# Kernel optimization log

Measured on AMD Instinct MI355X. Metric: run time of the kernel, lower is better.

The kernel has to match this reference:

```python
import jax, jax.numpy as jnp
import numpy as np

D_MODEL = 2048
NUM_Q_HEADS = 32
NUM_KV_HEADS = 8
HEAD_DIM = D_MODEL // NUM_Q_HEADS  # 64
DIM_KV = NUM_KV_HEADS * HEAD_DIM   # 512
ROPE_THETA = 500000.0
B, T = 1, 2048


def setup_inputs() -> dict:
    key = jax.random.key(0)
    ks = jax.random.split(key, 7)
    f = lambda k, shape, scale: (jax.random.normal(k, shape, jnp.float32) * scale)
    return {
        "q_embs": f(ks[0], (B, T, D_MODEL), 1.0),
        "k_embs": f(ks[1], (B, T, D_MODEL), 1.0),
        "v_embs": f(ks[2], (B, T, D_MODEL), 1.0),
        "w_q": f(ks[3], (D_MODEL, D_MODEL), 0.02),
        "w_k": f(ks[4], (D_MODEL, DIM_KV), 0.02),
        "w_v": f(ks[5], (D_MODEL, DIM_KV), 0.02),
        "w_o": f(ks[6], (D_MODEL, D_MODEL), 0.02),
    }


def _rope(x):
    # x: (B, H, T, D). Llama-style interleaved rotary embedding.
    Tn, D = x.shape[-2], x.shape[-1]
    inv_freq = 1.0 / (ROPE_THETA ** (jnp.arange(0, D, 2, dtype=jnp.float32) / D))  # (D/2,)
    ang = jnp.arange(Tn, dtype=jnp.float32)[:, None] * inv_freq[None, :]  # (T, D/2)
    cos, sin = jnp.cos(ang), jnp.sin(ang)
    x1, x2 = x[..., ::2], x[..., 1::2]
    # interleave rotated pairs back into last dim
    out = jnp.stack([x1 * cos - x2 * sin, x1 * sin + x2 * cos], axis=-1)
    return out.reshape(x.shape)


def reference(q_embs, k_embs, v_embs, w_q, w_k, w_v, w_o):
    Bn, Tn, _ = q_embs.shape
    # projections, then split heads: (B, T, H*D) -> (B, H, T, D)
    q = (q_embs @ w_q).reshape(Bn, Tn, NUM_Q_HEADS, HEAD_DIM).transpose(0, 2, 1, 3)
    k = (k_embs @ w_k).reshape(Bn, Tn, NUM_KV_HEADS, HEAD_DIM).transpose(0, 2, 1, 3)
    v = (v_embs @ w_v).reshape(Bn, Tn, NUM_KV_HEADS, HEAD_DIM).transpose(0, 2, 1, 3)
    q = _rope(q)
    k = _rope(k)
    # GQA: repeat each kv head n_rep consecutive times (matches torch expand+rearrange)
    n_rep = NUM_Q_HEADS // NUM_KV_HEADS
    k = jnp.repeat(k, n_rep, axis=1)
    v = jnp.repeat(v, n_rep, axis=1)
    scores = jnp.einsum("bhqd,bhkd->bhqk", q, k) * (HEAD_DIM ** -0.5)
    causal = jnp.tril(jnp.ones((Tn, Tn), dtype=bool))
    scores = jnp.where(causal, scores, -jnp.inf)
    wei = jax.nn.softmax(scores, axis=-1)
    out = jnp.einsum("bhqk,bhkd->bhqd", wei, v)
    out = out.transpose(0, 2, 1, 3).reshape(Bn, Tn, NUM_Q_HEADS * HEAD_DIM)
    return out @ w_o
```

## Files before the change

### kernel.cpp

```cpp
#include <hip/hip_runtime.h>
#include <hip/hip_bf16.h>
#include <cstdint>

#define D_MODEL 2048
#define T_SEQ   2048
#define NQH     32
#define NKVH    8
#define HD      64
#define DIM_KV  512

typedef __attribute__((ext_vector_type(8))) __bf16 bf16x8;
typedef __attribute__((ext_vector_type(4))) float  f32x4;
typedef __attribute__((ext_vector_type(4))) unsigned int u32x4;
typedef unsigned short ushort_t;

#define NEG_BIG (-1e30f)
#define AS1 __attribute__((address_space(1)))
#define AS3 __attribute__((address_space(3)))

__device__ __forceinline__ float bf2f(unsigned int u) {
    union { unsigned int i; float f; } v; v.i = u << 16; return v.f;
}
__device__ __forceinline__ ushort_t f2bf(float f) {
    __hip_bfloat16 h = __float2bfloat16(f);
    return *reinterpret_cast<ushort_t*>(&h);
}
__device__ __forceinline__ void gll16(const ushort_t* g, ushort_t* l) {
    __builtin_amdgcn_global_load_lds((const AS1 void*)g, (AS3 void*)l, 16, 0, 0);
}

__global__ __launch_bounds__(256) void conv_bf16(const float* __restrict__ X,
                                                 ushort_t* __restrict__ E, int n) {
    int i8 = (blockIdx.x * 256 + threadIdx.x) * 8;
    if (i8 >= n) return;
    f32x4 a = *(const f32x4*)(X + i8);
    f32x4 b = *(const f32x4*)(X + i8 + 4);
    u32x4 r;
    r.x = (unsigned)f2bf(a.x) | ((unsigned)f2bf(a.y) << 16);
    r.y = (unsigned)f2bf(a.z) | ((unsigned)f2bf(a.w) << 16);
    r.z = (unsigned)f2bf(b.x) | ((unsigned)f2bf(b.y) << 16);
    r.w = (unsigned)f2bf(b.z) | ((unsigned)f2bf(b.w) << 16);
    *(u32x4*)(E + i8) = r;
}

__global__ __launch_bounds__(256) void transpose_w(const float* __restrict__ W,
                                                   ushort_t* __restrict__ Wt,
                                                   int K, int N) {
    __shared__ ushort_t tile[64][65];
    int n0 = blockIdx.x * 64;
    int k0 = blockIdx.y * 64;
    int tid = threadIdx.x;
#pragma unroll
    for (int ii = 0; ii < 16; ii++) {
        int idx = tid + ii * 256;
        int r = idx >> 6, c = idx & 63;
        tile[r][c] = f2bf(W[(size_t)(k0 + r) * N + n0 + c]);
    }
    __syncthreads();
#pragma unroll
    for (int ii = 0; ii < 16; ii++) {
        int idx = tid + ii * 256;
        int r = idx >> 6, c = idx & 63;
        Wt[(size_t)(n0 + r) * K + k0 + c] = tile[c][r];
    }
}

__global__ __launch_bounds__(256) void transpose_v(const ushort_t* __restrict__ V,
                                                   ushort_t* __restrict__ Vt) {
    __shared__ ushort_t tile[64][65];
    int h  = blockIdx.y;
    int j0 = blockIdx.x * 64;
    int tid = threadIdx.x;
#pragma unroll
    for (int ii = 0; ii < 16; ii++) {
        int idx = tid + ii * 256;
        int r = idx >> 6, c = idx & 63;
        tile[r][c] = V[(size_t)(j0 + r) * DIM_KV + h * HD + c];
    }
    __syncthreads();
#pragma unroll
    for (int ii = 0; ii < 16; ii++) {
        int idx = tid + ii * 256;
        int r = idx >> 6, c = idx & 63;
        Vt[((size_t)h * HD + r) * T_SEQ + j0 + c] = tile[c][r];
    }
}

template <int OF32>
__global__ __launch_bounds__(256) void gemm128x64(const ushort_t* __restrict__ A,
                                                  const ushort_t* __restrict__ Bt,
                                                  void* __restrict__ C,
                                                  int M, int N, int K) {
    __shared__ ushort_t As[2][128][32];
    __shared__ ushort_t Bs[2][64][32];
    int tid  = threadIdx.x;
    int lane = tid & 63;
    int wave = tid >> 6;
    int m0 = blockIdx.y * 128;
    int n0 = blockIdx.x * 64;
    int wm = (wave >> 1) * 64;
    int wn = (wave & 1) * 32;
    int lrow = tid >> 2;
    int lcol = (tid & 3) * 8;

    f32x4 acc[4][2];
#pragma unroll
    for (int i = 0; i < 4; i++)
#pragma unroll
        for (int j = 0; j < 2; j++) acc[i][j] = (f32x4){0.f, 0.f, 0.f, 0.f};

    const int mrow = lane & 15;
    const int kq   = (lane >> 4) * 8;

    gll16(A  + (size_t)(m0 + lrow) * K + lcol,      &As[0][lrow][lcol]);
    gll16(A  + (size_t)(m0 + 64 + lrow) * K + lcol, &As[0][64 + lrow][lcol]);
    gll16(Bt + (size_t)(n0 + lrow) * K + lcol,      &Bs[0][lrow][lcol]);
    __syncthreads();

    int nk  = K >> 5;
    int cur = 0;
    for (int t = 0; t < nk; t++) {
        if (t + 1 < nk) {
            int k1 = (t + 1) << 5;
            gll16(A  + (size_t)(m0 + lrow) * K + k1 + lcol,      &As[cur ^ 1][lrow][lcol]);
            gll16(A  + (size_t)(m0 + 64 + lrow) * K + k1 + lcol, &As[cur ^ 1][64 + lrow][lcol]);
            gll16(Bt + (size_t)(n0 + lrow) * K + k1 + lcol,      &Bs[cur ^ 1][lrow][lcol]);
        }
        bf16x8 afr[4], bfr[2];
#pragma unroll
        for (int i = 0; i < 4; i++) afr[i] = *(const bf16x8*)&As[cur][wm + i * 16 + mrow][kq];
#pragma unroll
        for (int j = 0; j < 2; j++) bfr[j] = *(const bf16x8*)&Bs[cur][wn + j * 16 + mrow][kq];
#pragma unroll
        for (int i = 0; i < 4; i++)
#pragma unroll
            for (int j = 0; j < 2; j++)
                acc[i][j] = __builtin_amdgcn_mfma_f32_16x16x32_bf16(afr[i], bfr[j], acc[i][j], 0, 0, 0);
        __syncthreads();
        cur ^= 1;
    }

    int crow = (lane >> 4) * 4;
    int ccol = lane & 15;
#pragma unroll
    for (int i = 0; i < 4; i++)
#pragma unroll
        for (int j = 0; j < 2; j++) {
            int col = n0 + wn + j * 16 + ccol;
#pragma unroll
            for (int r = 0; r < 4; r++) {
                int row = m0 + wm + i * 16 + crow + r;
                if (OF32) ((float*)C)[(size_t)row * N + col] = acc[i][j][r];
                else      ((ushort_t*)C)[(size_t)row * N + col] = f2bf(acc[i][j][r]);
            }
        }
}

__global__ __launch_bounds__(256) void gemm64kv(const ushort_t* __restrict__ Ek,
                                                const ushort_t* __restrict__ wkT,
                                                const ushort_t* __restrict__ Ev,
                                                const ushort_t* __restrict__ wvT,
                                                ushort_t* __restrict__ Kb,
                                                ushort_t* __restrict__ Vb,
                                                int K) {
    __shared__ ushort_t As[2][64][32];
    __shared__ ushort_t Bs[2][64][32];
    int tid  = threadIdx.x;
    int lane = tid & 63;
    int wave = tid >> 6;
    bool isV = blockIdx.x >= 8;
    const ushort_t* A  = isV ? Ev : Ek;
    const ushort_t* Bt = isV ? wvT : wkT;
    ushort_t* C        = isV ? Vb : Kb;
    int m0 = blockIdx.y * 64;
    int n0 = (blockIdx.x & 7) * 64;
    int wm = (wave >> 1) * 32;
    int wn = (wave & 1) * 32;
    int lrow = tid >> 2;
    int lcol = (tid & 3) * 8;

    f32x4 acc[2][2];
#pragma unroll
    for (int i = 0; i < 2; i++)
#pragma unroll
        for (int j = 0; j < 2; j++) acc[i][j] = (f32x4){0.f, 0.f, 0.f, 0.f};

    const int mrow = lane & 15;
    const int kq   = (lane >> 4) * 8;

    gll16(A  + (size_t)(m0 + lrow) * K + lcol, &As[0][lrow][lcol]);
    gll16(Bt + (size_t)(n0 + lrow) * K + lcol, &Bs[0][lrow][lcol]);
    __syncthreads();

    int nk  = K >> 5;
    int cur = 0;
    for (int t = 0; t < nk; t++) {
        if (t + 1 < nk) {
            int k1 = (t + 1) << 5;
            gll16(A  + (size_t)(m0 + lrow) * K + k1 + lcol, &As[cur ^ 1][lrow][lcol]);
            gll16(Bt + (size_t)(n0 + lrow) * K + k1 + lcol, &Bs[cur ^ 1][lrow][lcol]);
        }
        bf16x8 afr[2], bfr[2];
#pragma unroll
        for (int i = 0; i < 2; i++) afr[i] = *(const bf16x8*)&As[cur][wm + i * 16 + mrow][kq];
#pragma unroll
        for (int j = 0; j < 2; j++) bfr[j] = *(const bf16x8*)&Bs[cur][wn + j * 16 + mrow][kq];
#pragma unroll
        for (int i = 0; i < 2; i++)
#pragma unroll
            for (int j = 0; j < 2; j++)
                acc[i][j] = __builtin_amdgcn_mfma_f32_16x16x32_bf16(afr[i], bfr[j], acc[i][j], 0, 0, 0);
        __syncthreads();
        cur ^= 1;
    }

    int crow = (lane >> 4) * 4;
    int ccol = lane & 15;
#pragma unroll
    for (int i = 0; i < 2; i++)
#pragma unroll
        for (int j = 0; j < 2; j++) {
            int col = n0 + wn + j * 16 + ccol;
#pragma unroll
            for (int r = 0; r < 4; r++) {
                int row = m0 + wm + i * 16 + crow + r;
                C[(size_t)row * DIM_KV + col] = f2bf(acc[i][j][r]);
            }
        }
}

__global__ void rope_kernel(ushort_t* __restrict__ X, int T, int cols) {
    int idx = blockIdx.x * blockDim.x + threadIdx.x;
    int ppr = cols >> 1;
    if (idx >= T * ppr) return;
    int t = idx / ppr;
    int j = idx - t * ppr;
    int i = j & 31;
    int col = ((j >> 5) << 6) + (i << 1);
    float inv = expf(-(float)i * (13.122363377404328f / 32.0f));
    float ang = (float)t * inv;
    float c = cosf(ang), s = sinf(ang);
    size_t base = (size_t)t * cols + col;
    float x1 = bf2f((unsigned int)X[base]);
    float x2 = bf2f((unsigned int)X[base + 1]);
    X[base]     = f2bf(x1 * c - x2 * s);
    X[base + 1] = f2bf(x1 * s + x2 * c);
}

__global__ __launch_bounds__(256) void attn_mfma(const ushort_t* __restrict__ Q,
                                                 const ushort_t* __restrict__ Kb,
                                                 const ushort_t* __restrict__ Vt,
                                                 ushort_t* __restrict__ Ob) {
    __shared__ ushort_t Qs[64][72];
    __shared__ ushort_t Ks[64][72];
    __shared__ ushort_t Vs[64][72];
    __shared__ ushort_t Ps[64][72];

    int tid  = threadIdx.x;
    int lane = tid & 63;
    int wave = tid >> 6;
    int h    = blockIdx.x;
    int hk   = h >> 2;
    int y    = blockIdx.y;
    int qt   = (y < 8) ? y : (y < 16) ? 23 - y : (y < 24) ? y : 55 - y;
    int q0   = qt * 64;
    int l15  = lane & 15;
    int quad = lane >> 4;
    int kq   = quad * 8;

    int r = tid >> 3;
    int c = (tid & 7) * 8;

    *(u32x4*)&Qs[r][c]      = *(const u32x4*)(Q + (size_t)(q0 + r) * D_MODEL + h * HD + c);
    *(u32x4*)&Qs[r + 32][c] = *(const u32x4*)(Q + (size_t)(q0 + r + 32) * D_MODEL + h * HD + c);
    __syncthreads();
    bf16x8 aq0 = *(const bf16x8*)&Qs[wave * 16 + l15][kq];
    bf16x8 aq1 = *(const bf16x8*)&Qs[wave * 16 + l15][kq + 32];

    f32x4 oacc[4];
    float l_i[4];
#pragma unroll
    for (int i = 0; i < 4; i++) {
        oacc[i] = (f32x4){0.f, 0.f, 0.f, 0.f};
        l_i[i] = 0.f;
    }

    u32x4 kr0, kr1, vr0, vr1;
    {
        kr0 = *(const u32x4*)(Kb + (size_t)(0 + r) * DIM_KV + hk * HD + c);
        kr1 = *(const u32x4*)(Kb + (size_t)(32 + r) * DIM_KV + hk * HD + c);
        vr0 = *(const u32x4*)(Vt + ((size_t)hk * HD + r) * T_SEQ + 0 + c);
        vr1 = *(const u32x4*)(Vt + ((size_t)hk * HD + r + 32) * T_SEQ + 0 + c);
    }

    int ntiles = qt + 1;
    for (int jt = 0; jt < ntiles; jt++) {
        __syncthreads();
        *(u32x4*)&Ks[r][c]      = kr0;
        *(u32x4*)&Ks[r + 32][c] = kr1;
        *(u32x4*)&Vs[r][c]      = vr0;
        *(u32x4*)&Vs[r + 32][c] = vr1;
        __syncthreads();
        if (jt + 1 < ntiles) {
            int j0 = (jt + 1) * 64;
            kr0 = *(const u32x4*)(Kb + (size_t)(j0 + r) * DIM_KV + hk * HD + c);
            kr1 = *(const u32x4*)(Kb + (size_t)(j0 + r + 32) * DIM_KV + hk * HD + c);
            vr0 = *(const u32x4*)(Vt + ((size_t)hk * HD + r) * T_SEQ + j0 + c);
            vr1 = *(const u32x4*)(Vt + ((size_t)hk * HD + r + 32) * T_SEQ + j0 + c);
        }

        f32x4 sacc[4];
#pragma unroll
        for (int ct = 0; ct < 4; ct++) {
            bf16x8 bk0 = *(const bf16x8*)&Ks[ct * 16 + l15][kq];
            bf16x8 bk1 = *(const bf16x8*)&Ks[ct * 16 + l15][kq + 32];
            sacc[ct] = __builtin_amdgcn_mfma_f32_16x16x32_bf16(aq0, bk0, (f32x4){0.f,0.f,0.f,0.f}, 0, 0, 0);
            sacc[ct] = __builtin_amdgcn_mfma_f32_16x16x32_bf16(aq1, bk1, sacc[ct], 0, 0, 0);
        }

        bool diag = (jt == ntiles - 1);
#pragma unroll
        for (int reg = 0; reg < 4; reg++) {
            int y2 = quad * 4 + reg;
            float sum = 0.f;
#pragma unroll
            for (int ct = 0; ct < 4; ct++) {
                float sv = sacc[ct][reg] * 0.125f;
                if (diag && (ct * 16 + l15 > wave * 16 + y2)) sv = NEG_BIG;
                float p = __expf(sv);
                sum += p;
                Ps[wave * 16 + y2][ct * 16 + l15] = f2bf(p);
            }
            l_i[reg] += sum;
        }

        bf16x8 ap0 = *(const bf16x8*)&Ps[wave * 16 + l15][kq];
        bf16x8 ap1 = *(const bf16x8*)&Ps[wave * 16 + l15][kq + 32];
#pragma unroll
        for (int dt = 0; dt < 4; dt++) {
            bf16x8 bv0 = *(const bf16x8*)&Vs[dt * 16 + l15][kq];
            bf16x8 bv1 = *(const bf16x8*)&Vs[dt * 16 + l15][kq + 32];
            oacc[dt] = __builtin_amdgcn_mfma_f32_16x16x32_bf16(ap0, bv0, oacc[dt], 0, 0, 0);
            oacc[dt] = __builtin_amdgcn_mfma_f32_16x16x32_bf16(ap1, bv1, oacc[dt], 0, 0, 0);
        }
    }

#pragma unroll
    for (int reg = 0; reg < 4; reg++) {
        float tot = l_i[reg];
#pragma unroll
        for (int off = 1; off < 16; off <<= 1) tot += __shfl_xor(tot, off, 64);
        float inv = (tot > 0.f) ? 1.0f / tot : 0.f;
        int row = q0 + wave * 16 + quad * 4 + reg;
#pragma unroll
        for (int dt = 0; dt < 4; dt++) {
            Ob[(size_t)row * D_MODEL + h * HD + dt * 16 + l15] = f2bf(oacc[dt][reg] * inv);
        }
    }
}

extern "C" void kernel_launch(void* const* d_in, const int* in_sizes, int n_in,
                              void* d_out, int out_size, void* d_ws, size_t ws_size,
                              hipStream_t stream) {
    const float* q_embs = (const float*)d_in[0];
    const float* k_embs = (const float*)d_in[1];
    const float* v_embs = (const float*)d_in[2];
    const float* w_q = (const float*)d_in[3];
    const float* w_k = (const float*)d_in[4];
    const float* w_v = (const float*)d_in[5];
    const float* w_o = (const float*)d_in[6];
    float* out = (float*)d_out;

    const size_t M1 = (size_t)1024 * 1024;
    ushort_t* base = (ushort_t*)d_ws;
    ushort_t* Eq  = base + 0 * M1;
    ushort_t* Ek  = base + 0 * M1;
    ushort_t* Ab  = base + 0 * M1;
    ushort_t* wqT = base + 4 * M1;
    ushort_t* Ev  = base + 4 * M1;
    ushort_t* woT = base + 4 * M1;
    ushort_t* Qb  = base + 8 * M1;
    ushort_t* wkT = base + 12 * M1;
    ushort_t* Vt  = base + 12 * M1;
    ushort_t* wvT = base + 13 * M1;
    ushort_t* Kb  = base + 14 * M1;
    ushort_t* Vb  = base + 15 * M1;

    dim3 blk(256);
    const int NCONV = 2048 * 2048;

    transpose_w<<<dim3(32, 32), blk, 0, stream>>>(w_q, wqT, 2048, 2048);
    transpose_w<<<dim3(8, 32), blk, 0, stream>>>(w_k, wkT, 2048, 512);
    transpose_w<<<dim3(8, 32), blk, 0, stream>>>(w_v, wvT, 2048, 512);

    conv_bf16<<<NCONV / (256 * 8), blk, 0, stream>>>(q_embs, Eq, NCONV);
    gemm128x64<0><<<dim3(32, 16), blk, 0, stream>>>(Eq, wqT, Qb, 2048, 2048, 2048);

    conv_bf16<<<NCONV / (256 * 8), blk, 0, stream>>>(k_embs, Ek, NCONV);
    conv_bf16<<<NCONV / (256 * 8), blk, 0, stream>>>(v_embs, Ev, NCONV);
    gemm64kv<<<dim3(16, 32), blk, 0, stream>>>(Ek, wkT, Ev, wvT, Kb, Vb, 2048);

    rope_kernel<<<(2048 * 1024 + 255) / 256, blk, 0, stream>>>(Qb, 2048, 2048);
    rope_kernel<<<(2048 * 256 + 255) / 256, blk, 0, stream>>>(Kb, 2048, 512);

    transpose_v<<<dim3(32, 8), blk, 0, stream>>>(Vb, Vt);
    transpose_w<<<dim3(32, 32), blk, 0, stream>>>(w_o, woT, 2048, 2048);

    attn_mfma<<<dim3(32, 32), blk, 0, stream>>>(Qb, Kb, Vt, Ab);

    gemm128x64<1><<<dim3(32, 16), blk, 0, stream>>>(Ab, woT, out, 2048, 2048, 2048);
}
```

Baseline: 304.5 us.

## Fuse QKV projections into one GEMM with in-kernel fp32-to-bf16 conversion

Replaces the separate activation conversion kernels and the Q and K/V GEMMs with a single 48x32-block GEMM. It reads fp32 activations directly, converts them to bf16 in registers and stages them into LDS with double buffering. The three weight transposes and the two RoPE launches are each merged into one kernel. This removes the bf16 activation round-trip through memory and several launches. In exchange the Q projection now uses 64x64 tiles instead of 128x64, and the activation loads go through registers rather than direct global-to-LDS loads.

```diff
diff --git a/kernel.cpp b/kernel.cpp
--- a/kernel.cpp
+++ b/kernel.cpp
@@ -25,22 +25,46 @@
     __hip_bfloat16 h = __float2bfloat16(f);
     return *reinterpret_cast<ushort_t*>(&h);
 }
-__device__ __forceinline__ void gll16(const ushort_t* g, ushort_t* l) {
-    __builtin_amdgcn_global_load_lds((const AS1 void*)g, (AS3 void*)l, 16, 0, 0);
-}
-
-__global__ __launch_bounds__(256) void conv_bf16(const float* __restrict__ X,
-                                                 ushort_t* __restrict__ E, int n) {
-    int i8 = (blockIdx.x * 256 + threadIdx.x) * 8;
-    if (i8 >= n) return;
-    f32x4 a = *(const f32x4*)(X + i8);
-    f32x4 b = *(const f32x4*)(X + i8 + 4);
+__device__ __forceinline__ u32x4 pack8(f32x4 a, f32x4 b) {
     u32x4 r;
     r.x = (unsigned)f2bf(a.x) | ((unsigned)f2bf(a.y) << 16);
     r.y = (unsigned)f2bf(a.z) | ((unsigned)f2bf(a.w) << 16);
     r.z = (unsigned)f2bf(b.x) | ((unsigned)f2bf(b.y) << 16);
     r.w = (unsigned)f2bf(b.z) | ((unsigned)f2bf(b.w) << 16);
-    *(u32x4*)(E + i8) = r;
+    return r;
+}
+__device__ __forceinline__ void gll16(const ushort_t* g, ushort_t* l) {
+    __builtin_amdgcn_global_load_lds((const AS1 void*)g, (AS3 void*)l, 16, 0, 0);
+}
+
+__global__ __launch_bounds__(256) void transpose_w3(const float* __restrict__ Wq,
+                                                    const float* __restrict__ Wk,
+                                                    const float* __restrict__ Wv,
+                                                    ushort_t* __restrict__ WqT,
+                                                    ushort_t* __restrict__ WkT,
+                                                    ushort_t* __restrict__ WvT) {
+    __shared__ ushort_t tile[64][65];
+    int bx = blockIdx.x;
+    const float* W; ushort_t* Wt; int N, n0;
+    if (bx < 32)      { W = Wq; Wt = WqT; N = 2048; n0 = bx * 64; }
+    else if (bx < 40) { W = Wk; Wt = WkT; N = 512;  n0 = (bx - 32) * 64; }
+    else              { W = Wv; Wt = WvT; N = 512;  n0 = (bx - 40) * 64; }
+    const int K = 2048;
+    int k0 = blockIdx.y * 64;
+    int tid = threadIdx.x;
+#pragma unroll
+    for (int ii = 0; ii < 16; ii++) {
+        int idx = tid + ii * 256;
+        int r = idx >> 6, c = idx & 63;
+        tile[r][c] = f2bf(W[(size_t)(k0 + r) * N + n0 + c]);
+    }
+    __syncthreads();
+#pragma unroll
+    for (int ii = 0; ii < 16; ii++) {
+        int idx = tid + ii * 256;
+        int r = idx >> 6, c = idx & 63;
+        Wt[(size_t)(n0 + r) * K + k0 + c] = tile[c][r];
+    }
 }
 
 __global__ __launch_bounds__(256) void transpose_w(const float* __restrict__ W,
@@ -84,6 +108,91 @@
         int r = idx >> 6, c = idx & 63;
         Vt[((size_t)h * HD + r) * T_SEQ + j0 + c] = tile[c][r];
     }
+}
+
+__global__ __launch_bounds__(256, 6) void gemm_qkv(const float* __restrict__ Aq,
+                                                   const float* __restrict__ Ak,
+                                                   const float* __restrict__ Av,
+                                                   const ushort_t* __restrict__ wqT,
+                                                   const ushort_t* __restrict__ wkT,
+                                                   const ushort_t* __restrict__ wvT,
+                                                   ushort_t* __restrict__ Qb,
+                                                   ushort_t* __restrict__ Kb,
+                                                   ushort_t* __restrict__ Vb) {
+    __shared__ ushort_t As[2][64][32];
+    __shared__ ushort_t Bs[2][64][32];
+    int tid  = threadIdx.x;
+    int lane = tid & 63;
+    int wave = tid >> 6;
+    int bx   = blockIdx.x;
+    const float* A; const ushort_t* Bt; ushort_t* C; int n0, ldc;
+    if (bx < 32)      { A = Aq; Bt = wqT; C = Qb; n0 = bx * 64;        ldc = D_MODEL; }
+    else if (bx < 40) { A = Ak; Bt = wkT; C = Kb; n0 = (bx - 32) * 64; ldc = DIM_KV; }
+    else              { A = Av; Bt = wvT; C = Vb; n0 = (bx - 40) * 64; ldc = DIM_KV; }
+    const int K = 2048;
+    int m0 = blockIdx.y * 64;
+    int wm = (wave >> 1) * 32;
+    int wn = (wave & 1) * 32;
+    int arow = tid >> 2;
+    int acol = (tid & 3) * 8;
+
+    f32x4 acc[2][2];
+#pragma unroll
+    for (int i = 0; i < 2; i++)
+#pragma unroll
+        for (int j = 0; j < 2; j++) acc[i][j] = (f32x4){0.f, 0.f, 0.f, 0.f};
+
+    const int mrow = lane & 15;
+    const int kq   = (lane >> 4) * 8;
+    const float* Arow = A + (size_t)(m0 + arow) * K + acol;
+    const ushort_t* Brow = Bt + (size_t)(n0 + arow) * K + acol;
+
+    f32x4 pa0 = *(const f32x4*)(Arow);
+    f32x4 pa1 = *(const f32x4*)(Arow + 4);
+    gll16(Brow, &Bs[0][arow][acol]);
+    *(u32x4*)&As[0][arow][acol] = pack8(pa0, pa1);
+    __syncthreads();
+
+    int cur = 0;
+#pragma unroll 1
+    for (int t = 0; t < 64; t++) {
+        bool more = (t + 1) < 64;
+        if (more) {
+            int k1 = (t + 1) << 5;
+            pa0 = *(const f32x4*)(Arow + k1);
+            pa1 = *(const f32x4*)(Arow + k1 + 4);
+            gll16(Brow + k1, &Bs[cur ^ 1][arow][acol]);
+        }
+        bf16x8 afr[2], bfr[2];
+#pragma unroll
+        for (int i = 0; i < 2; i++) afr[i] = *(const bf16x8*)&As[cur][wm + i * 16 + mrow][kq];
+#pragma unroll
+        for (int j = 0; j < 2; j++) bfr[j] = *(const bf16x8*)&Bs[cur][wn + j * 16 + mrow][kq];
+#pragma unroll
+        for (int i = 0; i < 2; i++)
+#pragma unroll
+            for (int j = 0; j < 2; j++)
+                acc[i][j] = __builtin_amdgcn_mfma_f32_16x16x32_bf16(afr[i], bfr[j], acc[i][j], 0, 0, 0);
+        if (more) {
+            *(u32x4*)&As[cur ^ 1][arow][acol] = pack8(pa0, pa1);
+        }
+        __syncthreads();
+        cur ^= 1;
+    }
+
+    int crow = (lane >> 4) * 4;
+    int ccol = lane & 15;
+#pragma unroll
+    for (int i = 0; i < 2; i++)
+#pragma unroll
+        for (int j = 0; j < 2; j++) {
+            int col = n0 + wn + j * 16 + ccol;
+#pragma unroll
+            for (int r = 0; r < 4; r++) {
+                int row = m0 + wm + i * 16 + crow + r;
+                C[(size_t)row * ldc + col] = f2bf(acc[i][j][r]);
+            }
+        }
 }
 
 template <int OF32>
@@ -156,83 +265,18 @@
         }
 }
 
-__global__ __launch_bounds__(256) void gemm64kv(const ushort_t* __restrict__ Ek,
-                                                const ushort_t* __restrict__ wkT,
-                                                const ushort_t* __restrict__ Ev,
-                                                const ushort_t* __restrict__ wvT,
-                                                ushort_t* __restrict__ Kb,
-                                                ushort_t* __restrict__ Vb,
-                                                int K) {
-    __shared__ ushort_t As[2][64][32];
-    __shared__ ushort_t Bs[2][64][32];
-    int tid  = threadIdx.x;
-    int lane = tid & 63;
-    int wave = tid >> 6;
-    bool isV = blockIdx.x >= 8;
-    const ushort_t* A  = isV ? Ev : Ek;
-    const ushort_t* Bt = isV ? wvT : wkT;
-    ushort_t* C        = isV ? Vb : Kb;
-    int m0 = blockIdx.y * 64;
-    int n0 = (blockIdx.x & 7) * 64;
-    int wm = (wave >> 1) * 32;
-    int wn = (wave & 1) * 32;
-    int lrow = tid >> 2;
-    int lcol = (tid & 3) * 8;
-
-    f32x4 acc[2][2];
-#pragma unroll
-    for (int i = 0; i < 2; i++)
-#pragma unroll
-        for (int j = 0; j < 2; j++) acc[i][j] = (f32x4){0.f, 0.f, 0.f, 0.f};
-
-    const int mrow = lane & 15;
-    const int kq   = (lane >> 4) * 8;
-
-    gll16(A  + (size_t)(m0 + lrow) * K + lcol, &As[0][lrow][lcol]);
-    gll16(Bt + (size_t)(n0 + lrow) * K + lcol, &Bs[0][lrow][lcol]);
-    __syncthreads();
-
-    int nk  = K >> 5;
-    int cur = 0;
-    for (int t = 0; t < nk; t++) {
-        if (t + 1 < nk) {
-            int k1 = (t + 1) << 5;
-            gll16(A  + (size_t)(m0 + lrow) * K + k1 + lcol, &As[cur ^ 1][lrow][lcol]);
-            gll16(Bt + (size_t)(n0 + lrow) * K + k1 + lcol, &Bs[cur ^ 1][lrow][lcol]);
-        }
-        bf16x8 afr[2], bfr[2];
-#pragma unroll
-        for (int i = 0; i < 2; i++) afr[i] = *(const bf16x8*)&As[cur][wm + i * 16 + mrow][kq];
-#pragma unroll
-        for (int j = 0; j < 2; j++) bfr[j] = *(const bf16x8*)&Bs[cur][wn + j * 16 + mrow][kq];
-#pragma unroll
-        for (int i = 0; i < 2; i++)
-#pragma unroll
-            for (int j = 0; j < 2; j++)
-                acc[i][j] = __builtin_amdgcn_mfma_f32_16x16x32_bf16(afr[i], bfr[j], acc[i][j], 0, 0, 0);
-        __syncthreads();
-        cur ^= 1;
-    }
-
-    int crow = (lane >> 4) * 4;
-    int ccol = lane & 15;
-#pragma unroll
-    for (int i = 0; i < 2; i++)
-#pragma unroll
-        for (int j = 0; j < 2; j++) {
-            int col = n0 + wn + j * 16 + ccol;
-#pragma unroll
-            for (int r = 0; r < 4; r++) {
-                int row = m0 + wm + i * 16 + crow + r;
-                C[(size_t)row * DIM_KV + col] = f2bf(acc[i][j][r]);
-            }
-        }
-}
-
-__global__ void rope_kernel(ushort_t* __restrict__ X, int T, int cols) {
+__global__ void rope_fused(ushort_t* __restrict__ Qb, ushort_t* __restrict__ Kb) {
+    const int NQ = T_SEQ * (D_MODEL / 2);
+    const int NK = T_SEQ * (DIM_KV / 2);
     int idx = blockIdx.x * blockDim.x + threadIdx.x;
+    ushort_t* X; int cols;
+    if (idx < NQ) { X = Qb; cols = D_MODEL; }
+    else {
+        idx -= NQ;
+        if (idx >= NK) return;
+        X = Kb; cols = DIM_KV;
+    }
     int ppr = cols >> 1;
-    if (idx >= T * ppr) return;
     int t = idx / ppr;
     int j = idx - t * ppr;
     int i = j & 31;
@@ -373,35 +417,25 @@
 
     const size_t M1 = (size_t)1024 * 1024;
     ushort_t* base = (ushort_t*)d_ws;
-    ushort_t* Eq  = base + 0 * M1;
-    ushort_t* Ek  = base + 0 * M1;
-    ushort_t* Ab  = base + 0 * M1;
-    ushort_t* wqT = base + 4 * M1;
-    ushort_t* Ev  = base + 4 * M1;
-    ushort_t* woT = base + 4 * M1;
-    ushort_t* Qb  = base + 8 * M1;
-    ushort_t* wkT = base + 12 * M1;
-    ushort_t* Vt  = base + 12 * M1;
-    ushort_t* wvT = base + 13 * M1;
-    ushort_t* Kb  = base + 14 * M1;
-    ushort_t* Vb  = base + 15 * M1;
+    ushort_t* wqT = base + 0 * M1;
+    ushort_t* woT = base + 0 * M1;
+    ushort_t* wkT = base + 4 * M1;
+    ushort_t* Vt  = base + 4 * M1;
+    ushort_t* wvT = base + 5 * M1;
+    ushort_t* Qb  = base + 6 * M1;
+    ushort_t* Kb  = base + 10 * M1;
+    ushort_t* Vb  = base + 11 * M1;
+    ushort_t* Ab  = base + 12 * M1;
 
     dim3 blk(256);
-    const int NCONV = 2048 * 2048;
-
-    transpose_w<<<dim3(32, 32), blk, 0, stream>>>(w_q, wqT, 2048, 2048);
-    transpose_w<<<dim3(8, 32), blk, 0, stream>>>(w_k, wkT, 2048, 512);
-    transpose_w<<<dim3(8, 32), blk, 0, stream>>>(w_v, wvT, 2048, 512);
-
-    conv_bf16<<<NCONV / (256 * 8), blk, 0, stream>>>(q_embs, Eq, NCONV);
-    gemm128x64<0><<<dim3(32, 16), blk, 0, stream>>>(Eq, wqT, Qb, 2048, 2048, 2048);
-
-    conv_bf16<<<NCONV / (256 * 8), blk, 0, stream>>>(k_embs, Ek, NCONV);
-    conv_bf16<<<NCONV / (256 * 8), blk, 0, stream>>>(v_embs, Ev, NCONV);
-    gemm64kv<<<dim3(16, 32), blk, 0, stream>>>(Ek, wkT, Ev, wvT, Kb, Vb, 2048);
-
-    rope_kernel<<<(2048 * 1024 + 255) / 256, blk, 0, stream>>>(Qb, 2048, 2048);
-    rope_kernel<<<(2048 * 256 + 255) / 256, blk, 0, stream>>>(Kb, 2048, 512);
+
+    transpose_w3<<<dim3(48, 32), blk, 0, stream>>>(w_q, w_k, w_v, wqT, wkT, wvT);
+
+    gemm_qkv<<<dim3(48, 32), blk, 0, stream>>>(q_embs, k_embs, v_embs,
+                                               wqT, wkT, wvT, Qb, Kb, Vb);
+
+    const int NROPE = T_SEQ * (D_MODEL / 2) + T_SEQ * (DIM_KV / 2);
+    rope_fused<<<(NROPE + 255) / 256, blk, 0, stream>>>(Qb, Kb);
 
     transpose_v<<<dim3(32, 8), blk, 0, stream>>>(Vb, Vt);
     transpose_w<<<dim3(32, 32), blk, 0, stream>>>(w_o, woT, 2048, 2048);
```

Result: no change. 304.3 us (-0.1%).
